# Kernel optimization log

Measured on AMD Instinct MI355X. Metric: run time of the kernel, lower is better.

Reference implementation:

```python
import jax, jax.numpy as jnp
import numpy as np
from functools import partial

N = 9
NN = N * N  # 81 cells
BTS = 4096
HID = 100


def build_constraint_mask():
    idx = np.arange(NN)
    r, c = idx // N, idx % N
    b = (r // 3) * 3 + (c // 3)
    row = (r[:, None] == r[None, :]).astype(np.float32)
    col = (c[:, None] == c[None, :]).astype(np.float32)
    box = (b[:, None] == b[None, :]).astype(np.float32)
    return jnp.asarray(np.stack([row, col, box], axis=1))  # [81, 3, 81]


def setup_inputs() -> dict:
    key = jax.random.key(0)
    k1, k2, k3, k4 = jax.random.split(key, 4)
    vals = jax.random.randint(k1, (BTS, NN), 0, N)
    filled = jax.random.uniform(k2, (BTS, NN)) < 0.4
    x = jax.nn.one_hot(vals, N, dtype=jnp.float32) * filled[:, :, None].astype(jnp.float32)
    W1 = jax.random.normal(k3, (HID, 3 * N), dtype=jnp.float32) * 0.1
    W2 = jax.random.normal(k4, (N, HID), dtype=jnp.float32) * 0.1
    return {"x": x, "W1": W1, "W2": W2, "constraint_mask": build_constraint_mask()}


def _sudoku_forward(x, W1, W2, cmask):
    bts = x.shape[0]
    b_idx = jnp.arange(bts)

    def step(carry, _):
        x, x_pred = carry
        # constraints[b,i,k,v] = sum_j cmask[i,k,j] * x[b,j,v]  -> [b,81,3,9]
        constraints = jnp.einsum('ikj,bjv->bikv', cmask, x)
        f = constraints.reshape(bts, NN, 3 * N)            # [b,81,27]
        h = jax.nn.relu(jnp.einsum('bif,hf->bih', f, W1))  # [b,81,100]
        y = jnp.einsum('bih,vh->biv', h, W2)               # [b,81,9]
        probs = jax.nn.softmax(y, axis=-1)
        empty = x.sum(-1) == 0                             # [b,81]
        x_pred = jnp.where(empty[..., None], probs, x_pred)
        s = jnp.where(empty[..., None], probs, 0.0)
        score = s.max(-1)                                  # [b,81]
        pos = jnp.argmax(s, -1)                            # [b,81]
        mmax = jnp.argmax(score, -1)                       # [b] best cell
        has_empty = empty.any(-1)                          # [b]
        sel_pos = pos[b_idx, mmax]
        newv = jnp.where(has_empty, 1.0, x[b_idx, mmax, sel_pos])
        x = x.at[b_idx, mmax, sel_pos].set(newv)
        return (x, x_pred), None

    # Original loops min_empty (max empties over batch) times; running the full
    # NN=81 steps is equivalent since iterations past a board's fill are no-ops.
    (x, x_pred), _ = jax.lax.scan(step, (x, x), None, length=NN)
    return x_pred, x


@jax.jit
def reference(x, W1, W2, constraint_mask):
    return _sudoku_forward(x, W1, W2, constraint_mask)
```

## Files before the change

### kernel.cpp

```cpp
#include <hip/hip_runtime.h>

#define TPB 256


__device__ __forceinline__ int affected_cell(int slot, int fr, int fc) {
    if (slot < 9)  return fr * 9 + slot;
    if (slot < 18) return (slot - 9) * 9 + fc;
    int r0 = (fr / 3) * 3, c0 = (fc / 3) * 3;
    int dr = fr - r0, dc = fc - c0;
    int rA = r0 + (dr == 0 ? 1 : 0), rB = r0 + (dr == 2 ? 1 : 2);
    int cA = c0 + (dc == 0 ? 1 : 0), cB = c0 + (dc == 2 ? 1 : 2);
    int k = slot - 18;
    return ((k < 2) ? rA : rB) * 9 + ((k & 1) ? cB : cA);
}

__device__ __forceinline__ void do_F(int slot, int q, int cell,
    const double* __restrict__ H1, const double* __restrict__ W2Td,
    double* __restrict__ pbuf)
{
    int r = cell / 9, c = cell - 9 * r;
    int bx = (r / 3) * 3 + c / 3;
    const double* Hr = H1 + r * 101;
    const double* Hc = H1 + (9 + c) * 101;
    const double* Hb = H1 + (18 + bx) * 101;
    double acc[9];
#pragma unroll
    for (int v = 0; v < 9; v++) acc[v] = 0.0;
    const int j0 = q * 12;
#pragma unroll
    for (int jj = 0; jj < 12; jj++) {
        int j = j0 + jj;
        if (j < 100) {
            double h = Hr[j] + Hc[j] + Hb[j];
            h = h > 0.0 ? h : 0.0;
            const double* w = W2Td + j * 9;
#pragma unroll
            for (int v = 0; v < 9; v++) acc[v] = fma(h, w[v], acc[v]);
        }
    }
    double* pb = pbuf + (slot * 9 + q) * 9;
#pragma unroll
    for (int v = 0; v < 9; v++) pb[v] = acc[v];
}

__device__ __forceinline__ void do_C(int slot, int v, int cell,
    const double* __restrict__ pbuf, double* __restrict__ ybuf,
    double* __restrict__ pexp, float* __restrict__ outp,
    double* __restrict__ score_l, int* __restrict__ pos_l)
{
    double y = 0.0;
#pragma unroll
    for (int q = 0; q < 9; q++) y += pbuf[(slot * 9 + q) * 9 + v];
    ybuf[slot * 9 + v] = y;
    __builtin_amdgcn_wave_barrier();
    double m = ybuf[slot * 9 + 0];
#pragma unroll
    for (int v2 = 1; v2 < 9; v2++) m = fmax(m, ybuf[slot * 9 + v2]);
    pexp[slot * 9 + v] = exp(y - m);
    __builtin_amdgcn_wave_barrier();
    if (v == 0) {
        double sum = 0.0;
#pragma unroll
        for (int v2 = 0; v2 < 9; v2++) sum += pexp[slot * 9 + v2];
        double inv = 1.0 / sum;
        double best = -1.0; int bv = 0;
#pragma unroll
        for (int v2 = 0; v2 < 9; v2++) {
            double pr = pexp[slot * 9 + v2] * inv;
            outp[cell * 9 + v2] = (float)pr;
            if (pr > best) { best = pr; bv = v2; }
        }
        score_l[cell] = best;
        pos_l[cell] = bv;
    }
}

__global__ __launch_bounds__(TPB, 4) void sudoku_kernel(
    const float* __restrict__ x_in,
    const float* __restrict__ W1,
    const float* __restrict__ W2,
    float* __restrict__ out,
    int nb)
{
    const int b = blockIdx.x;
    const int t = threadIdx.x;

    __shared__ float  xs[729];
    __shared__ double W2Td[100 * 9];
    __shared__ double cnt[27 * 12];
    __shared__ double H1[27 * 101];
    __shared__ double pbuf[22 * 9 * 9];
    __shared__ double ybuf[22 * 9];
    __shared__ double pexp[22 * 9];
    __shared__ double score_l[81];
    __shared__ int    pos_l[81];
    __shared__ int    bc_cell;

    float* outp = out + (size_t)b * 729;
    const float* xb = x_in + (size_t)b * 729;
    for (int i = t; i < 729; i += TPB) { float v = xb[i]; xs[i] = v; outp[i] = v; }
    for (int i = t; i < 900; i += TPB) { int v = i / 100, j = i - 100 * v; W2Td[j * 9 + v] = (double)W2[i]; }
    __syncthreads();

    if (t < 81) {
        float s = 0.f;
#pragma unroll
        for (int v = 0; v < 9; v++) s += xs[t * 9 + v];
        score_l[t] = (s == 0.f) ? 0.0 : -1.0;
        pos_l[t] = 0;
    }
    for (int o = t; o < 243; o += TPB) {
        int g = o / 9, v = o - 9 * g;
        float s = 0.f;
        if (g < 9) {
            int base = g * 9;
#pragma unroll
            for (int k = 0; k < 9; k++) s += xs[(base + k) * 9 + v];
        } else if (g < 18) {
            int c = g - 9;
#pragma unroll
            for (int k = 0; k < 9; k++) s += xs[(c + 9 * k) * 9 + v];
        } else {
            int bx = g - 18;
            int base = (bx / 3) * 27 + (bx % 3) * 3;
#pragma unroll
            for (int k = 0; k < 9; k++) s += xs[(base + (k / 3) * 9 + (k % 3)) * 9 + v];
        }
        cnt[g * 12 + v] = (double)s;
    }
    __syncthreads();

    for (int o = t; o < 2700; o += TPB) {
        int g = o / 100, j = o - 100 * g;
        int type = (g >= 18) ? 2 : (g >= 9 ? 1 : 0);
        const float* w = W1 + j * 27 + type * 9;
        const double* cc = cnt + g * 12;
        double s = 0.0;
#pragma unroll
        for (int v = 0; v < 9; v++) s = fma((double)w[v], cc[v], s);
        H1[g * 101 + j] = s;
    }
    int myflag = (t < 81) ? (score_l[t] == 0.0) : 0;
    int ne = __syncthreads_count(myflag);

    for (int c0 = 0; c0 < 81; c0 += 22) {
        if (t < 198) {
            int slot = t % 22, q = t / 22;
            int cell = c0 + slot;
            if (cell < 81 && score_l[cell] >= 0.0)
                do_F(slot, q, cell, H1, W2Td, pbuf);
        }
        __syncthreads();
        {
            int w = t >> 6, l = t & 63;
            if (l < 63) {
                int sw = l / 9, v = l - 9 * sw;
                int slot = w * 7 + sw;
                int cell = c0 + slot;
                if (slot < 22 && cell < 81 && score_l[cell] >= 0.0)
                    do_C(slot, v, cell, pbuf, ybuf, pexp, outp, score_l, pos_l);
            }
        }
        __syncthreads();
    }

    for (int step = 0; step < ne; ++step) {
        if (t < 64) {
            double s = score_l[t]; int idx = t;
            if (t < 17) {
                double s2 = score_l[64 + t];
                if (s2 > s) { s = s2; idx = 64 + t; }
            }
#pragma unroll
            for (int off = 1; off < 64; off <<= 1) {
                double s2 = __shfl_xor(s, off);
                int    i2 = __shfl_xor(idx, off);
                if (s2 > s || (s2 == s && i2 < idx)) { s = s2; idx = i2; }
            }
            if (t == 0) {
                int cell = idx, bv = pos_l[cell];
                bc_cell = cell;
                xs[cell * 9 + bv] = 1.0f;
                score_l[cell] = -1.0;
                int r = cell / 9, c = cell - 9 * r;
                int bx = (r / 3) * 3 + c / 3;
                cnt[r * 12 + bv] += 1.0;
                cnt[(9 + c) * 12 + bv] += 1.0;
                cnt[(18 + bx) * 12 + bv] += 1.0;
            }
        }
        __syncthreads();
        const int fcell = bc_cell;
        const int fr = fcell / 9, fc = fcell - 9 * fr;
        const int fbx = (fr / 3) * 3 + fc / 3;

        for (int o = t; o < 300; o += TPB) {
            int gi = o / 100, j = o - 100 * gi;
            int g = (gi == 0) ? fr : (gi == 1) ? (9 + fc) : (18 + fbx);
            const float* w = W1 + j * 27 + gi * 9;
            const double* cc = cnt + g * 12;
            double s = 0.0;
#pragma unroll
            for (int v = 0; v < 9; v++) s = fma((double)w[v], cc[v], s);
            H1[g * 101 + j] = s;
        }
        __syncthreads();

        if (t < 198) {
            int slot = t % 22, q = t / 22;
            int cell = affected_cell(slot, fr, fc);
            if (score_l[cell] >= 0.0)
                do_F(slot, q, cell, H1, W2Td, pbuf);
        }
        __syncthreads();

        {
            int w = t >> 6, l = t & 63;
            if (l < 63) {
                int sw = l / 9, v = l - 9 * sw;
                int slot = w * 7 + sw;
                if (slot < 22) {
                    int cell = affected_cell(slot, fr, fc);
                    if (score_l[cell] >= 0.0)
                        do_C(slot, v, cell, pbuf, ybuf, pexp, outp, score_l, pos_l);
                }
            }
        }
        __syncthreads();
    }

    float* outx = out + (size_t)nb * 729 + (size_t)b * 729;
    for (int i = t; i < 729; i += TPB) outx[i] = xs[i];
}

extern "C" void kernel_launch(void* const* d_in, const int* in_sizes, int n_in,
                              void* d_out, int out_size, void* d_ws, size_t ws_size,
                              hipStream_t stream) {
    const float* x  = (const float*)d_in[0];
    const float* W1 = (const float*)d_in[1];
    const float* W2 = (const float*)d_in[2];
    int nb = in_sizes[0] / 729;
    (void)n_in; (void)out_size; (void)d_ws; (void)ws_size;
    sudoku_kernel<<<nb, TPB, 0, stream>>>(x, W1, W2, (float*)d_out, nb);
}
```

Baseline: 1.344 ms.

## Fuse FFN partial and softmax phases per wave, cut block barriers per step

```diff
diff --git a/kernel.cpp b/kernel.cpp
--- a/kernel.cpp
+++ b/kernel.cpp
@@ -14,9 +14,10 @@
     return ((k < 2) ? rA : rB) * 9 + ((k & 1) ? cB : cA);
 }
 
-__device__ __forceinline__ void do_F(int slot, int q, int cell,
+__device__ __forceinline__ void do_FC(int slot, int qv, int cell,
     const double* __restrict__ H1, const double* __restrict__ W2Td,
-    double* __restrict__ pbuf)
+    double* __restrict__ pbuf, double* __restrict__ ybuf,
+    float* __restrict__ outp, double* __restrict__ score_l, int* __restrict__ pos_l)
 {
     int r = cell / 9, c = cell - 9 * r;
     int bx = (r / 3) * 3 + c / 3;
@@ -26,7 +27,7 @@
     double acc[9];
 #pragma unroll
     for (int v = 0; v < 9; v++) acc[v] = 0.0;
-    const int j0 = q * 12;
+    const int j0 = qv * 12;
 #pragma unroll
     for (int jj = 0; jj < 12; jj++) {
         int j = j0 + jj;
@@ -38,44 +39,40 @@
             for (int v = 0; v < 9; v++) acc[v] = fma(h, w[v], acc[v]);
         }
     }
-    double* pb = pbuf + (slot * 9 + q) * 9;
+    double* pb = pbuf + (slot * 9 + qv) * 9;
 #pragma unroll
     for (int v = 0; v < 9; v++) pb[v] = acc[v];
-}
-
-__device__ __forceinline__ void do_C(int slot, int v, int cell,
-    const double* __restrict__ pbuf, double* __restrict__ ybuf,
-    double* __restrict__ pexp, float* __restrict__ outp,
-    double* __restrict__ score_l, int* __restrict__ pos_l)
-{
+    __builtin_amdgcn_wave_barrier();
     double y = 0.0;
 #pragma unroll
-    for (int q = 0; q < 9; q++) y += pbuf[(slot * 9 + q) * 9 + v];
-    ybuf[slot * 9 + v] = y;
+    for (int q2 = 0; q2 < 9; q2++) y += pbuf[(slot * 9 + q2) * 9 + qv];
+    ybuf[slot * 9 + qv] = y;
     __builtin_amdgcn_wave_barrier();
     double m = ybuf[slot * 9 + 0];
 #pragma unroll
     for (int v2 = 1; v2 < 9; v2++) m = fmax(m, ybuf[slot * 9 + v2]);
-    pexp[slot * 9 + v] = exp(y - m);
-    __builtin_amdgcn_wave_barrier();
-    if (v == 0) {
-        double sum = 0.0;
-#pragma unroll
-        for (int v2 = 0; v2 < 9; v2++) sum += pexp[slot * 9 + v2];
-        double inv = 1.0 / sum;
-        double best = -1.0; int bv = 0;
+    double e = exp(y - m);
+    __builtin_amdgcn_wave_barrier();
+    ybuf[slot * 9 + qv] = e;
+    __builtin_amdgcn_wave_barrier();
+    double p[9], sum = 0.0;
+#pragma unroll
+    for (int v2 = 0; v2 < 9; v2++) { p[v2] = ybuf[slot * 9 + v2]; sum += p[v2]; }
+    double inv = 1.0 / sum;
+    outp[cell * 9 + qv] = (float)(p[qv] * inv);
+    if (qv == 0) {
+        double best = -1.0; int bvv = 0;
 #pragma unroll
         for (int v2 = 0; v2 < 9; v2++) {
-            double pr = pexp[slot * 9 + v2] * inv;
-            outp[cell * 9 + v2] = (float)pr;
-            if (pr > best) { best = pr; bv = v2; }
+            double pr = p[v2] * inv;
+            if (pr > best) { best = pr; bvv = v2; }
         }
         score_l[cell] = best;
-        pos_l[cell] = bv;
-    }
-}
-
-__global__ __launch_bounds__(TPB, 4) void sudoku_kernel(
+        pos_l[cell] = bvv;
+    }
+}
+
+__global__ __launch_bounds__(TPB, 3) void sudoku_kernel(
     const float* __restrict__ x_in,
     const float* __restrict__ W1,
     const float* __restrict__ W2,
@@ -84,17 +81,17 @@
 {
     const int b = blockIdx.x;
     const int t = threadIdx.x;
+    const int W = t >> 6, l = t & 63;
+    const int ls = l / 9, qv = l - 9 * ls;
 
     __shared__ float  xs[729];
     __shared__ double W2Td[100 * 9];
-    __shared__ double cnt[27 * 12];
+    __shared__ double cnt[27 * 9];
     __shared__ double H1[27 * 101];
-    __shared__ double pbuf[22 * 9 * 9];
-    __shared__ double ybuf[22 * 9];
-    __shared__ double pexp[22 * 9];
+    __shared__ double pbuf[24 * 81];
+    __shared__ double ybuf[24 * 9];
     __shared__ double score_l[81];
     __shared__ int    pos_l[81];
-    __shared__ int    bc_cell;
 
     float* outp = out + (size_t)b * 729;
     const float* xb = x_in + (size_t)b * 729;
@@ -126,7 +123,7 @@
 #pragma unroll
             for (int k = 0; k < 9; k++) s += xs[(base + (k / 3) * 9 + (k % 3)) * 9 + v];
         }
-        cnt[g * 12 + v] = (double)s;
+        cnt[g * 9 + v] = (double)s;
     }
     __syncthreads();
 
@@ -134,7 +131,7 @@
         int g = o / 100, j = o - 100 * g;
         int type = (g >= 18) ? 2 : (g >= 9 ? 1 : 0);
         const float* w = W1 + j * 27 + type * 9;
-        const double* cc = cnt + g * 12;
+        const double* cc = cnt + g * 9;
         double s = 0.0;
 #pragma unroll
         for (int v = 0; v < 9; v++) s = fma((double)w[v], cc[v], s);
@@ -143,87 +140,61 @@
     int myflag = (t < 81) ? (score_l[t] == 0.0) : 0;
     int ne = __syncthreads_count(myflag);
 
-    for (int c0 = 0; c0 < 81; c0 += 22) {
-        if (t < 198) {
-            int slot = t % 22, q = t / 22;
+    for (int c0 = 0; c0 < 96; c0 += 24) {
+        if (l < 54) {
+            int slot = W * 6 + ls;
             int cell = c0 + slot;
             if (cell < 81 && score_l[cell] >= 0.0)
-                do_F(slot, q, cell, H1, W2Td, pbuf);
-        }
-        __syncthreads();
-        {
-            int w = t >> 6, l = t & 63;
-            if (l < 63) {
-                int sw = l / 9, v = l - 9 * sw;
-                int slot = w * 7 + sw;
-                int cell = c0 + slot;
-                if (slot < 22 && cell < 81 && score_l[cell] >= 0.0)
-                    do_C(slot, v, cell, pbuf, ybuf, pexp, outp, score_l, pos_l);
-            }
-        }
-        __syncthreads();
-    }
+                do_FC(slot, qv, cell, H1, W2Td, pbuf, ybuf, outp, score_l, pos_l);
+        }
+    }
+    __syncthreads();
 
     for (int step = 0; step < ne; ++step) {
-        if (t < 64) {
-            double s = score_l[t]; int idx = t;
-            if (t < 17) {
-                double s2 = score_l[64 + t];
-                if (s2 > s) { s = s2; idx = 64 + t; }
-            }
-#pragma unroll
-            for (int off = 1; off < 64; off <<= 1) {
-                double s2 = __shfl_xor(s, off);
-                int    i2 = __shfl_xor(idx, off);
-                if (s2 > s || (s2 == s && i2 < idx)) { s = s2; idx = i2; }
-            }
-            if (t == 0) {
-                int cell = idx, bv = pos_l[cell];
-                bc_cell = cell;
-                xs[cell * 9 + bv] = 1.0f;
-                score_l[cell] = -1.0;
-                int r = cell / 9, c = cell - 9 * r;
-                int bx = (r / 3) * 3 + c / 3;
-                cnt[r * 12 + bv] += 1.0;
-                cnt[(9 + c) * 12 + bv] += 1.0;
-                cnt[(18 + bx) * 12 + bv] += 1.0;
-            }
-        }
-        __syncthreads();
-        const int fcell = bc_cell;
-        const int fr = fcell / 9, fc = fcell - 9 * fr;
-        const int fbx = (fr / 3) * 3 + fc / 3;
+        double s = score_l[l]; int idx = l;
+        if (l < 17) {
+            double s2 = score_l[64 + l];
+            if (s2 > s) { s = s2; idx = 64 + l; }
+        }
+#pragma unroll
+        for (int off = 1; off < 64; off <<= 1) {
+            double s2 = __shfl_xor(s, off);
+            int    i2 = __shfl_xor(idx, off);
+            if (s2 > s || (s2 == s && i2 < idx)) { s = s2; idx = i2; }
+        }
+        const int fcell = idx;
+        const int bv = pos_l[fcell];
+        const int fr = fcell / 9, fcc = fcell - 9 * fr;
+        const int fbx = (fr / 3) * 3 + fcc / 3;
 
         for (int o = t; o < 300; o += TPB) {
             int gi = o / 100, j = o - 100 * gi;
-            int g = (gi == 0) ? fr : (gi == 1) ? (9 + fc) : (18 + fbx);
+            int g = (gi == 0) ? fr : (gi == 1) ? (9 + fcc) : (18 + fbx);
             const float* w = W1 + j * 27 + gi * 9;
-            const double* cc = cnt + g * 12;
-            double s = 0.0;
-#pragma unroll
-            for (int v = 0; v < 9; v++) s = fma((double)w[v], cc[v], s);
-            H1[g * 101 + j] = s;
+            const double* cc = cnt + g * 9;
+            double h = 0.0;
+#pragma unroll
+            for (int v = 0; v < 9; v++) {
+                double cv = cc[v] + (v == bv ? 1.0 : 0.0);
+                h = fma((double)w[v], cv, h);
+            }
+            H1[g * 101 + j] = h;
         }
         __syncthreads();
 
-        if (t < 198) {
-            int slot = t % 22, q = t / 22;
-            int cell = affected_cell(slot, fr, fc);
-            if (score_l[cell] >= 0.0)
-                do_F(slot, q, cell, H1, W2Td, pbuf);
-        }
-        __syncthreads();
-
-        {
-            int w = t >> 6, l = t & 63;
-            if (l < 63) {
-                int sw = l / 9, v = l - 9 * sw;
-                int slot = w * 7 + sw;
-                if (slot < 22) {
-                    int cell = affected_cell(slot, fr, fc);
-                    if (score_l[cell] >= 0.0)
-                        do_C(slot, v, cell, pbuf, ybuf, pexp, outp, score_l, pos_l);
-                }
+        if (t == 0) {
+            xs[fcell * 9 + bv] = 1.0f;
+            score_l[fcell] = -1.0;
+            cnt[fr * 9 + bv] += 1.0;
+            cnt[(9 + fcc) * 9 + bv] += 1.0;
+            cnt[(18 + fbx) * 9 + bv] += 1.0;
+        }
+        if (l < 54) {
+            int slot = W * 6 + ls;
+            if (slot < 22) {
+                int cell = affected_cell(slot, fr, fcc);
+                if (cell != fcell && score_l[cell] >= 0.0)
+                    do_FC(slot, qv, cell, H1, W2Td, pbuf, ybuf, outp, score_l, pos_l);
             }
         }
         __syncthreads();
```

Measured after the change: 1.338 ms. Within noise of the previous version (-0.4%).
